# Kernel optimization log

Measured on AMD Instinct MI355X. Metric: run time of the kernel, lower is better.

Reference implementation:

```python
import jax, jax.numpy as jnp
import numpy as np

N = 50000   # nodes
E = 800000  # edges
F = 256     # input features
H = 256     # hidden units
L = 128     # n_labels
EPS = 1e-5


def setup_inputs():
    key = jax.random.key(0)
    ks = jax.random.split(key, 17)
    s = 0.05
    return {
        "features": jax.random.normal(ks[0], (N, F), jnp.float32),
        "edge_vals": jax.random.uniform(ks[1], (E,), jnp.float32),
        "W1": jax.random.normal(ks[2], (F, H), jnp.float32) * s,
        "db1": jax.random.normal(ks[3], (H,), jnp.float32) * s,
        "b1": jax.random.normal(ks[4], (H,), jnp.float32) * s,
        "g1": jax.random.uniform(ks[5], (H,), jnp.float32, 0.5, 1.5),
        "be1": jax.random.normal(ks[6], (H,), jnp.float32) * s,
        "W2": jax.random.normal(ks[7], (H, H), jnp.float32) * s,
        "b2": jax.random.normal(ks[8], (H,), jnp.float32) * s,
        "g2": jax.random.uniform(ks[9], (H,), jnp.float32, 0.5, 1.5),
        "be2": jax.random.normal(ks[10], (H,), jnp.float32) * s,
        "Wf": jax.random.normal(ks[11], (H, L), jnp.float32) * s,
        "bf": jax.random.normal(ks[12], (L,), jnp.float32) * s,
        "edge_rows": jax.random.randint(ks[13], (E,), 0, N, jnp.int32),
        "edge_cols": jax.random.randint(ks[14], (E,), 0, N, jnp.int32),
        "idx": jax.random.randint(ks[15], (N // 2,), 0, N, jnp.int32),
    }


def _spmm(edge_vals, rows, cols, x):
    # out[i] = sum_{(i,j) in E} A[i,j] * x[j]  (COO sparse @ dense)
    return jax.ops.segment_sum(edge_vals[:, None] * x[cols], rows, num_segments=N)


def _bn(x, gamma, beta):
    # training-mode BatchNormalization: batch (population) stats over nodes
    m = jnp.mean(x, axis=0)
    v = jnp.var(x, axis=0)
    return (x - m) * jax.lax.rsqrt(v + EPS) * gamma + beta


def reference(features, edge_vals, W1, db1, b1, g1, be1, W2, b2, g2, be2, Wf, bf,
              edge_rows, edge_cols, idx):
    # layer 1 (Dense has bias only for l == 0)
    h = features @ W1 + db1
    h = _spmm(edge_vals, edge_rows, edge_cols, h) + b1
    h = jax.nn.relu(_bn(h, g1, be1))
    # layer 2 (no dense bias)
    h = h @ W2
    h = _spmm(edge_vals, edge_rows, edge_cols, h) + b2
    h = jax.nn.relu(_bn(h, g2, be2))
    # dropout = identity (deterministic baseline); final dense head
    out = h @ Wf + bf
    return out[idx]
```

## Files before the change

### kernel.cpp

```cpp
#include <hip/hip_runtime.h>
#include <stdint.h>

#define NN 50000
#define EE 800000
#define FF 256
#define HH 256
#define LL 128
#define SBLK 1024

typedef __bf16 bf16x8 __attribute__((ext_vector_type(8)));
typedef float  f32x4  __attribute__((ext_vector_type(4)));

typedef __attribute__((address_space(1))) unsigned int uint_as1;
typedef __attribute__((address_space(3))) unsigned int uint_as3;

__device__ __forceinline__ unsigned short f2bf(float f) {
  union { float f; unsigned int u; } v; v.f = f;
  unsigned int u = v.u;
  u += 0x7FFFu + ((u >> 16) & 1u);
  return (unsigned short)(u >> 16);
}

__device__ __forceinline__ float bf2f(unsigned short u) {
  union { unsigned int u; float f; } v;
  v.u = ((unsigned int)u) << 16;
  return v.f;
}

__device__ __forceinline__ f32x4 bf4_to_f32(ushort4 u) {
  f32x4 r;
  r.x = bf2f(u.x); r.y = bf2f(u.y); r.z = bf2f(u.z); r.w = bf2f(u.w);
  return r;
}

__device__ __forceinline__ void gload_lds16(const void* g, void* l) {
  __builtin_amdgcn_global_load_lds((const uint_as1*)g, (uint_as3*)l, 16, 0, 0);
}

__global__ __launch_bounds__(256) void k_casts(const float* __restrict__ features,
                                               unsigned short* __restrict__ Xb,
                                               const float* __restrict__ W1,
                                               unsigned short* __restrict__ W1t,
                                               const float* __restrict__ W2,
                                               unsigned short* __restrict__ W2t,
                                               const float* __restrict__ Wf,
                                               unsigned short* __restrict__ Wft,
                                               int* __restrict__ cnt,
                                               int* __restrict__ statz) {
  __shared__ float tl[64 * 65];
  int b = blockIdx.x, t = threadIdx.x;
  if (b < 12500) {
    int i = b * 256 + t;
    f32x4 x = ((const f32x4*)features)[i];
    ushort4 o;
    o.x = f2bf(x.x); o.y = f2bf(x.y); o.z = f2bf(x.z); o.w = f2bf(x.w);
    ((ushort4*)Xb)[i] = o;
  } else if (b < 12540) {
    const float* in;
    unsigned short* out;
    int Nin, k0, n0;
    if (b < 12516) {
      in = W1; out = W1t; Nin = HH;
      int tt = b - 12500; k0 = (tt >> 2) * 64; n0 = (tt & 3) * 64;
    } else if (b < 12532) {
      in = W2; out = W2t; Nin = HH;
      int tt = b - 12516; k0 = (tt >> 2) * 64; n0 = (tt & 3) * 64;
    } else {
      in = Wf; out = Wft; Nin = LL;
      int tt = b - 12532; k0 = (tt >> 1) * 64; n0 = (tt & 1) * 64;
    }
#pragma unroll
    for (int j = 0; j < 16; ++j) {
      int idx = j * 256 + t;
      int r = idx >> 6, c = idx & 63;
      tl[r * 65 + c] = in[(size_t)(k0 + r) * Nin + n0 + c];
    }
    __syncthreads();
#pragma unroll
    for (int j = 0; j < 16; ++j) {
      int idx = j * 256 + t;
      int r = idx >> 6, c = idx & 63;
      out[(size_t)(n0 + r) * HH + k0 + c] = f2bf(tl[c * 65 + r]);
    }
  } else if (b < 12589) {
    int base = (b - 12540) * 1024 + t * 4;
    if (base + 3 < NN) {
      int4 z = {0, 0, 0, 0};
      *(int4*)(cnt + base) = z;
    } else {
      for (int j = 0; j < 4; ++j)
        if (base + j < NN) cnt[base + j] = 0;
    }
  } else {
    for (int i = t; i < 4 * HH + 64; i += 256) statz[i] = 0;
  }
}

__global__ __launch_bounds__(256) void k_hist(const int* __restrict__ rows,
                                              int* __restrict__ cnt, int E) {
  int i = blockIdx.x * 256 + threadIdx.x;
  if (i < E) atomicAdd(&cnt[rows[i]], 1);
}

__global__ __launch_bounds__(256) void k_alloc(const int* __restrict__ cnt,
                                               int* __restrict__ cursor,
                                               int* __restrict__ total, int n) {
  int i = blockIdx.x * 256 + threadIdx.x;
  int lane = threadIdx.x & 63;
  int c = (i < n) ? cnt[i] : 0;
  int incl = c;
#pragma unroll
  for (int off = 1; off < 64; off <<= 1) {
    int v = __shfl_up(incl, off, 64);
    if (lane >= off) incl += v;
  }
  int excl = incl - c;
  int wtot = __shfl(incl, 63, 64);
  int base = 0;
  if (lane == 0) base = atomicAdd(total, wtot);
  base = __shfl(base, 0, 64);
  if (i < n) cursor[i] = base + excl;
}

__global__ __launch_bounds__(256) void k_fill(const int* __restrict__ rows,
                                              const int* __restrict__ cols,
                                              const float* __restrict__ vals,
                                              int* __restrict__ cursor,
                                              unsigned int* __restrict__ csr, int E) {
  int i = (blockIdx.x * 256 + threadIdx.x) * 2;
  if (i + 1 < E) {
    int2 r2 = *(const int2*)(rows + i);
    int2 c2 = *(const int2*)(cols + i);
    float2 v2 = *(const float2*)(vals + i);
    int p0 = atomicAdd(&cursor[r2.x], 1);
    csr[p0] = ((unsigned int)c2.x << 16) | (unsigned int)f2bf(v2.x);
    int p1 = atomicAdd(&cursor[r2.y], 1);
    csr[p1] = ((unsigned int)c2.y << 16) | (unsigned int)f2bf(v2.y);
  } else if (i < E) {
    int p = atomicAdd(&cursor[rows[i]], 1);
    csr[p] = ((unsigned int)cols[i] << 16) | (unsigned int)f2bf(vals[i]);
  }
}

__global__ __launch_bounds__(256) void k_spmm(const unsigned short* __restrict__ X,
                                              const int* __restrict__ endp,
                                              const int* __restrict__ cnt,
                                              const unsigned int* __restrict__ csr,
                                              unsigned short* __restrict__ Y, int n) {
  int row = blockIdx.x * 4 + (threadIdx.x >> 6);
  int lane = threadIdx.x & 63;
  if (row >= n) return;
  int e = endp[row];
  int s = e - cnt[row];
  f32x4 a0 = {0.f, 0.f, 0.f, 0.f};
  f32x4 a1 = a0, a2 = a0, a3 = a0;
  int p = s;
  int e4 = s + ((e - s) & ~3);
  for (; p < e4; p += 4) {
    unsigned int c0 = csr[p + 0], c1 = csr[p + 1], c2 = csr[p + 2], c3 = csr[p + 3];
    ushort4 x0 = ((const ushort4*)(X + (size_t)(c0 >> 16) * HH))[lane];
    ushort4 x1 = ((const ushort4*)(X + (size_t)(c1 >> 16) * HH))[lane];
    ushort4 x2 = ((const ushort4*)(X + (size_t)(c2 >> 16) * HH))[lane];
    ushort4 x3 = ((const ushort4*)(X + (size_t)(c3 >> 16) * HH))[lane];
    a0 += bf2f((unsigned short)c0) * bf4_to_f32(x0);
    a1 += bf2f((unsigned short)c1) * bf4_to_f32(x1);
    a2 += bf2f((unsigned short)c2) * bf4_to_f32(x2);
    a3 += bf2f((unsigned short)c3) * bf4_to_f32(x3);
  }
  for (; p < e; ++p) {
    unsigned int c0 = csr[p];
    ushort4 x0 = ((const ushort4*)(X + (size_t)(c0 >> 16) * HH))[lane];
    a0 += bf2f((unsigned short)c0) * bf4_to_f32(x0);
  }
  f32x4 a = (a0 + a1) + (a2 + a3);
  ushort4 o;
  o.x = f2bf(a.x); o.y = f2bf(a.y); o.z = f2bf(a.z); o.w = f2bf(a.w);
  ((ushort4*)(Y + (size_t)row * HH))[lane] = o;
}

__global__ __launch_bounds__(256) void k_bnstats(const unsigned short* __restrict__ X,
                                                 float* __restrict__ part, int n) {
  __shared__ float red[4][64][9];
  const int w = threadIdx.x >> 6, l = threadIdx.x & 63;
  f32x4 s = {0.f, 0.f, 0.f, 0.f}, s2 = {0.f, 0.f, 0.f, 0.f};
  for (int r = blockIdx.x * 4 + w; r < n; r += gridDim.x * 4) {
    f32x4 v = bf4_to_f32(((const ushort4*)(X + (size_t)r * HH))[l]);
    s += v;
    s2 += v * v;
  }
#pragma unroll
  for (int j = 0; j < 4; ++j) { red[w][l][j] = s[j]; red[w][l][4 + j] = s2[j]; }
  __syncthreads();
  if (threadIdx.x < 64) {
    int ll = threadIdx.x;
#pragma unroll
    for (int j = 0; j < 8; ++j) {
      float v = red[0][ll][j] + red[1][ll][j] + red[2][ll][j] + red[3][ll][j];
      int c = ll * 4 + (j & 3);
      part[((j < 4) ? 0 : (SBLK * 256)) + blockIdx.x * 256 + c] = v;
    }
  }
}

__global__ __launch_bounds__(256) void k_bnred(const float* __restrict__ part,
                                               float* __restrict__ sums) {
  int c = threadIdx.x;
  int stat = blockIdx.x >> 3, chunk = blockIdx.x & 7;
  const float* p = part + stat * (SBLK * 256) + chunk * 128 * 256;
  float s0 = 0.f, s1 = 0.f, s2 = 0.f, s3 = 0.f;
  for (int b = 0; b < 128; b += 4) {
    s0 += p[(b + 0) * 256 + c];
    s1 += p[(b + 1) * 256 + c];
    s2 += p[(b + 2) * 256 + c];
    s3 += p[(b + 3) * 256 + c];
  }
  atomicAdd(&sums[stat * HH + c], (s0 + s1) + (s2 + s3));
}

__global__ __launch_bounds__(256) void k_bnrc(const unsigned short* __restrict__ X,
                                              const float* __restrict__ sums,
                                              const float* __restrict__ g,
                                              const float* __restrict__ be,
                                              unsigned short* __restrict__ out, int n4) {
  __shared__ float sc[HH], sh[HH];
  int t = threadIdx.x;
  {
    float inv = 1.f / (float)NN;
    float mean = sums[t] * inv;
    float var = sums[HH + t] * inv - mean * mean;
    float s = g[t] * rsqrtf(var + 1e-5f);
    sc[t] = s;
    sh[t] = be[t] - mean * s;
  }
  __syncthreads();
  for (int i = blockIdx.x * 256 + t; i < n4; i += gridDim.x * 256) {
    f32x4 x = bf4_to_f32(((const ushort4*)X)[i]);
    int c0 = (i * 4) & (HH - 1);
    ushort4 o;
    o.x = f2bf(fmaxf(x.x * sc[c0 + 0] + sh[c0 + 0], 0.f));
    o.y = f2bf(fmaxf(x.y * sc[c0 + 1] + sh[c0 + 1], 0.f));
    o.z = f2bf(fmaxf(x.z * sc[c0 + 2] + sh[c0 + 2], 0.f));
    o.w = f2bf(fmaxf(x.w * sc[c0 + 3] + sh[c0 + 3], 0.f));
    ((ushort4*)out)[i] = o;
  }
}

__global__ __launch_bounds__(256) void k_bnrc_pack(const unsigned short* __restrict__ X,
                                                   const float* __restrict__ sums,
                                                   const float* __restrict__ g,
                                                   const float* __restrict__ be,
                                                   const int* __restrict__ idx,
                                                   unsigned short* __restrict__ out) {
  __shared__ float sc[HH], sh[HH];
  int t = threadIdx.x;
  {
    float inv = 1.f / (float)NN;
    float mean = sums[t] * inv;
    float var = sums[HH + t] * inv - mean * mean;
    float s = g[t] * rsqrtf(var + 1e-5f);
    sc[t] = s;
    sh[t] = be[t] - mean * s;
  }
  __syncthreads();
  int i = blockIdx.x * 256 + t;
  int orow = i >> 6;
  int c0 = (i & 63) * 4;
  int irow = idx[orow];
  f32x4 x = bf4_to_f32(*(const ushort4*)(X + (size_t)irow * HH + c0));
  ushort4 o;
  o.x = f2bf(fmaxf(x.x * sc[c0 + 0] + sh[c0 + 0], 0.f));
  o.y = f2bf(fmaxf(x.y * sc[c0 + 1] + sh[c0 + 1], 0.f));
  o.z = f2bf(fmaxf(x.z * sc[c0 + 2] + sh[c0 + 2], 0.f));
  o.w = f2bf(fmaxf(x.w * sc[c0 + 3] + sh[c0 + 3], 0.f));
  ((ushort4*)out)[i] = o;
}

template <int OUTB>
__global__ __launch_bounds__(256, 3) void k_gemm(const unsigned short* __restrict__ A,
                                                 const unsigned short* __restrict__ Bt,
                                                 const float* __restrict__ bias,
                                                 void* __restrict__ Cv,
                                                 int M, int K, int Nn) {
  __shared__ unsigned short lA[128 * 64];
  __shared__ unsigned short lB[128 * 64];
  const int tid = threadIdx.x;
  const int wave = tid >> 6, lane = tid & 63;
  const int m0 = blockIdx.x * 128, n0 = blockIdx.y * 128;
  const int wm = (wave >> 1) * 64, wn = (wave & 1) * 64;
  const int lhi = lane >> 4, llo = lane & 15;

  const int srow = lane >> 3;
  const int scol = (lane & 7) * 8;
  const unsigned short *pA[4], *pB[4];
#pragma unroll
  for (int j = 0; j < 4; ++j) {
    int base = (wave * 4 + j) * 8 + srow;
    int ar = m0 + base;
    ar = ar < M ? ar : 0;
    pA[j] = A + (size_t)ar * K + scol;
    pB[j] = Bt + (size_t)(n0 + base) * K + scol;
  }

  f32x4 zero = {0.f, 0.f, 0.f, 0.f};
  f32x4 acc[4][4];
#pragma unroll
  for (int i = 0; i < 4; ++i)
#pragma unroll
    for (int j = 0; j < 4; ++j) acc[i][j] = zero;

  for (int k0 = 0; k0 < K; k0 += 64) {
#pragma unroll
    for (int j = 0; j < 4; ++j) {
      gload_lds16(pA[j] + k0, lA + (wave * 4 + j) * 8 * 64);
      gload_lds16(pB[j] + k0, lB + (wave * 4 + j) * 8 * 64);
    }
    __syncthreads();
    bf16x8 af[2][4], bfv[2][4];
#pragma unroll
    for (int ks = 0; ks < 2; ++ks) {
#pragma unroll
      for (int mt = 0; mt < 4; ++mt)
        af[ks][mt] = *(const bf16x8*)(lA + (wm + mt * 16 + llo) * 64 + ks * 32 + lhi * 8);
#pragma unroll
      for (int nt = 0; nt < 4; ++nt)
        bfv[ks][nt] = *(const bf16x8*)(lB + (wn + nt * 16 + llo) * 64 + ks * 32 + lhi * 8);
    }
#pragma unroll
    for (int ks = 0; ks < 2; ++ks)
#pragma unroll
      for (int mt = 0; mt < 4; ++mt)
#pragma unroll
        for (int nt = 0; nt < 4; ++nt)
          acc[mt][nt] = __builtin_amdgcn_mfma_f32_16x16x32_bf16(af[ks][mt], bfv[ks][nt], acc[mt][nt], 0, 0, 0);
    __syncthreads();
  }

#pragma unroll
  for (int nt = 0; nt < 4; ++nt) {
    int cn = n0 + wn + nt * 16 + llo;
    float bv = bias ? bias[cn] : 0.f;
#pragma unroll
    for (int mt = 0; mt < 4; ++mt) {
      int cm0 = m0 + wm + mt * 16 + lhi * 4;
#pragma unroll
      for (int r = 0; r < 4; ++r) {
        int cm = cm0 + r;
        if (cm < M) {
          float v = acc[mt][nt][r] + bv;
          if (OUTB)
            ((unsigned short*)Cv)[(size_t)cm * Nn + cn] = f2bf(v);
          else
            ((float*)Cv)[(size_t)cm * Nn + cn] = v;
        }
      }
    }
  }
}

extern "C" void kernel_launch(void* const* d_in, const int* in_sizes, int n_in,
                              void* d_out, int out_size, void* d_ws, size_t ws_size,
                              hipStream_t stream) {
  const float* features = (const float*)d_in[0];
  const float* edge_vals = (const float*)d_in[1];
  const float* W1 = (const float*)d_in[2];
  const float* db1 = (const float*)d_in[3];
  const float* g1 = (const float*)d_in[5];
  const float* be1 = (const float*)d_in[6];
  const float* W2 = (const float*)d_in[7];
  const float* g2 = (const float*)d_in[9];
  const float* be2 = (const float*)d_in[10];
  const float* Wf = (const float*)d_in[11];
  const float* bfb = (const float*)d_in[12];
  const int* erows = (const int*)d_in[13];
  const int* ecols = (const int*)d_in[14];
  const int* idx = (const int*)d_in[15];
  const int M3 = in_sizes[15];
  (void)n_in; (void)out_size; (void)ws_size;

  char* ws = (char*)d_ws;
  size_t off = 0;
  auto alloc = [&](size_t bytes) -> void* {
    void* p = (void*)(ws + off);
    off += (bytes + 255) & ~(size_t)255;
    return p;
  };
  unsigned short* Xb = (unsigned short*)alloc((size_t)NN * HH * 2);
  unsigned short* Ab = (unsigned short*)alloc((size_t)NN * HH * 2);
  unsigned short* Yb = (unsigned short*)alloc((size_t)NN * HH * 2);
  unsigned short* Pb = (unsigned short*)alloc((size_t)25000 * HH * 2);
  unsigned short* W1t = (unsigned short*)alloc((size_t)FF * HH * 2);
  unsigned short* W2t = (unsigned short*)alloc((size_t)HH * HH * 2);
  unsigned short* Wft = (unsigned short*)alloc((size_t)HH * LL * 2);
  int* cursor = (int*)alloc((size_t)NN * 4);
  int* cnt = (int*)alloc((size_t)NN * 4);
  unsigned int* csr = (unsigned int*)alloc((size_t)EE * 4);
  float* part = (float*)alloc((size_t)2 * SBLK * 256 * 4);
  float* stats = (float*)alloc(4 * HH * 4 + 256);
  float* sums1 = stats;
  float* sums2 = stats + 2 * HH;
  int* total = (int*)(stats + 4 * HH);

  k_casts<<<12590, 256, 0, stream>>>(features, Xb, W1, W1t, W2, W2t, Wf, Wft,
                                     cnt, (int*)stats);

  k_hist<<<(EE + 255) / 256, 256, 0, stream>>>(erows, cnt, EE);
  k_alloc<<<(NN + 255) / 256, 256, 0, stream>>>(cnt, cursor, total, NN);
  k_fill<<<(EE / 2 + 255) / 256, 256, 0, stream>>>(erows, ecols, edge_vals, cursor, csr, EE);

  k_gemm<1><<<dim3((NN + 127) / 128, HH / 128), 256, 0, stream>>>(Xb, W1t, db1, Ab, NN, FF, HH);
  k_spmm<<<(NN + 3) / 4, 256, 0, stream>>>(Ab, cursor, cnt, csr, Yb, NN);
  k_bnstats<<<SBLK, 256, 0, stream>>>(Yb, part, NN);
  k_bnred<<<16, 256, 0, stream>>>(part, sums1);
  k_bnrc<<<2048, 256, 0, stream>>>(Yb, sums1, g1, be1, Xb, NN * HH / 4);

  k_gemm<1><<<dim3((NN + 127) / 128, HH / 128), 256, 0, stream>>>(Xb, W2t, nullptr, Ab, NN, HH, HH);
  k_spmm<<<(NN + 3) / 4, 256, 0, stream>>>(Ab, cursor, cnt, csr, Yb, NN);
  k_bnstats<<<SBLK, 256, 0, stream>>>(Yb, part, NN);
  k_bnred<<<16, 256, 0, stream>>>(part, sums2);
  k_bnrc_pack<<<(M3 * 64) / 256, 256, 0, stream>>>(Yb, sums2, g2, be2, idx, Pb);

  k_gemm<0><<<dim3((M3 + 127) / 128, LL / 128), 256, 0, stream>>>(Pb, Wft, bfb, d_out, M3, HH, LL);
}
```

Measured before the change: 463.8 us.

## Fuse histogram into setup kernel and overlap CSR fill with layer-1 GEMM

The edge-row histogram moves into the cast/transpose setup kernel, and the zeroing of cnt and stats is replaced by hipMemsetAsync calls. The CSR fill is merged into the layer-1 GEMM launch: odd blocks scatter edges with a grid-stride loop while even blocks compute GEMM tiles. This cuts launch count and lets the atomic-bound scatter overlap the MFMA work. The risk is contention between the two block types and an interleaved block mapping that may hurt GEMM scheduling. The fill also loses its two-edges-per-thread vectorized loads.

```diff
diff --git a/kernel.cpp b/kernel.cpp
--- a/kernel.cpp
+++ b/kernel.cpp
@@ -37,37 +37,41 @@
   __builtin_amdgcn_global_load_lds((const uint_as1*)g, (uint_as3*)l, 16, 0, 0);
 }
 
-__global__ __launch_bounds__(256) void k_casts(const float* __restrict__ features,
+__global__ __launch_bounds__(256) void k_setup(const int* __restrict__ erows,
+                                               int* __restrict__ cnt,
+                                               const float* __restrict__ features,
                                                unsigned short* __restrict__ Xb,
                                                const float* __restrict__ W1,
                                                unsigned short* __restrict__ W1t,
                                                const float* __restrict__ W2,
                                                unsigned short* __restrict__ W2t,
                                                const float* __restrict__ Wf,
-                                               unsigned short* __restrict__ Wft,
-                                               int* __restrict__ cnt,
-                                               int* __restrict__ statz) {
+                                               unsigned short* __restrict__ Wft) {
   __shared__ float tl[64 * 65];
   int b = blockIdx.x, t = threadIdx.x;
-  if (b < 12500) {
+  if (b < 3125) {
     int i = b * 256 + t;
+    if (i < EE) atomicAdd(&cnt[erows[i]], 1);
+  } else if (b < 15625) {
+    int i = (b - 3125) * 256 + t;
     f32x4 x = ((const f32x4*)features)[i];
     ushort4 o;
     o.x = f2bf(x.x); o.y = f2bf(x.y); o.z = f2bf(x.z); o.w = f2bf(x.w);
     ((ushort4*)Xb)[i] = o;
-  } else if (b < 12540) {
+  } else {
+    int tt = b - 15625;
     const float* in;
     unsigned short* out;
     int Nin, k0, n0;
-    if (b < 12516) {
+    if (tt < 16) {
       in = W1; out = W1t; Nin = HH;
-      int tt = b - 12500; k0 = (tt >> 2) * 64; n0 = (tt & 3) * 64;
-    } else if (b < 12532) {
+      k0 = (tt >> 2) * 64; n0 = (tt & 3) * 64;
+    } else if (tt < 32) {
       in = W2; out = W2t; Nin = HH;
-      int tt = b - 12516; k0 = (tt >> 2) * 64; n0 = (tt & 3) * 64;
+      tt -= 16; k0 = (tt >> 2) * 64; n0 = (tt & 3) * 64;
     } else {
       in = Wf; out = Wft; Nin = LL;
-      int tt = b - 12532; k0 = (tt >> 1) * 64; n0 = (tt & 1) * 64;
+      tt -= 32; k0 = (tt >> 1) * 64; n0 = (tt & 1) * 64;
     }
 #pragma unroll
     for (int j = 0; j < 16; ++j) {
@@ -82,24 +86,7 @@
       int r = idx >> 6, c = idx & 63;
       out[(size_t)(n0 + r) * HH + k0 + c] = f2bf(tl[c * 65 + r]);
     }
-  } else if (b < 12589) {
-    int base = (b - 12540) * 1024 + t * 4;
-    if (base + 3 < NN) {
-      int4 z = {0, 0, 0, 0};
-      *(int4*)(cnt + base) = z;
-    } else {
-      for (int j = 0; j < 4; ++j)
-        if (base + j < NN) cnt[base + j] = 0;
-    }
-  } else {
-    for (int i = t; i < 4 * HH + 64; i += 256) statz[i] = 0;
-  }
-}
-
-__global__ __launch_bounds__(256) void k_hist(const int* __restrict__ rows,
-                                              int* __restrict__ cnt, int E) {
-  int i = blockIdx.x * 256 + threadIdx.x;
-  if (i < E) atomicAdd(&cnt[rows[i]], 1);
+  }
 }
 
 __global__ __launch_bounds__(256) void k_alloc(const int* __restrict__ cnt,
@@ -122,23 +109,88 @@
   if (i < n) cursor[i] = base + excl;
 }
 
-__global__ __launch_bounds__(256) void k_fill(const int* __restrict__ rows,
-                                              const int* __restrict__ cols,
-                                              const float* __restrict__ vals,
-                                              int* __restrict__ cursor,
-                                              unsigned int* __restrict__ csr, int E) {
-  int i = (blockIdx.x * 256 + threadIdx.x) * 2;
-  if (i + 1 < E) {
-    int2 r2 = *(const int2*)(rows + i);
-    int2 c2 = *(const int2*)(cols + i);
-    float2 v2 = *(const float2*)(vals + i);
-    int p0 = atomicAdd(&cursor[r2.x], 1);
-    csr[p0] = ((unsigned int)c2.x << 16) | (unsigned int)f2bf(v2.x);
-    int p1 = atomicAdd(&cursor[r2.y], 1);
-    csr[p1] = ((unsigned int)c2.y << 16) | (unsigned int)f2bf(v2.y);
-  } else if (i < E) {
-    int p = atomicAdd(&cursor[rows[i]], 1);
-    csr[p] = ((unsigned int)cols[i] << 16) | (unsigned int)f2bf(vals[i]);
+__global__ __launch_bounds__(256, 3) void k_l1(const unsigned short* __restrict__ A,
+                                               const unsigned short* __restrict__ Bt,
+                                               const float* __restrict__ bias,
+                                               unsigned short* __restrict__ C,
+                                               int M, int K, int Nn,
+                                               const int* __restrict__ rows,
+                                               const int* __restrict__ cols,
+                                               const float* __restrict__ vals,
+                                               int* __restrict__ cursor,
+                                               unsigned int* __restrict__ csr, int E) {
+  __shared__ unsigned short lA[128 * 64];
+  __shared__ unsigned short lB[128 * 64];
+  const int b = blockIdx.x;
+  const int tid = threadIdx.x;
+  if (b & 1) {
+    for (int i = (b >> 1) * 256 + tid; i < E; i += 782 * 256) {
+      int p = atomicAdd(&cursor[rows[i]], 1);
+      csr[p] = ((unsigned int)cols[i] << 16) | (unsigned int)f2bf(vals[i]);
+    }
+    return;
+  }
+  const int gb = b >> 1;
+  const int m0 = (gb % 391) * 128, n0 = (gb / 391) * 128;
+  const int wave = tid >> 6, lane = tid & 63;
+  const int wm = (wave >> 1) * 64, wn = (wave & 1) * 64;
+  const int lhi = lane >> 4, llo = lane & 15;
+  const int srow = lane >> 3;
+  const int scol = (lane & 7) * 8;
+  const unsigned short *pA[4], *pB[4];
+#pragma unroll
+  for (int j = 0; j < 4; ++j) {
+    int base = (wave * 4 + j) * 8 + srow;
+    int ar = m0 + base;
+    ar = ar < M ? ar : 0;
+    pA[j] = A + (size_t)ar * K + scol;
+    pB[j] = Bt + (size_t)(n0 + base) * K + scol;
+  }
+  f32x4 zero = {0.f, 0.f, 0.f, 0.f};
+  f32x4 acc[4][4];
+#pragma unroll
+  for (int i = 0; i < 4; ++i)
+#pragma unroll
+    for (int j = 0; j < 4; ++j) acc[i][j] = zero;
+  for (int k0 = 0; k0 < K; k0 += 64) {
+#pragma unroll
+    for (int j = 0; j < 4; ++j) {
+      gload_lds16(pA[j] + k0, lA + (wave * 4 + j) * 8 * 64);
+      gload_lds16(pB[j] + k0, lB + (wave * 4 + j) * 8 * 64);
+    }
+    __syncthreads();
+    bf16x8 af[2][4], bfv[2][4];
+#pragma unroll
+    for (int ks = 0; ks < 2; ++ks) {
+#pragma unroll
+      for (int mt = 0; mt < 4; ++mt)
+        af[ks][mt] = *(const bf16x8*)(lA + (wm + mt * 16 + llo) * 64 + ks * 32 + lhi * 8);
+#pragma unroll
+      for (int nt = 0; nt < 4; ++nt)
+        bfv[ks][nt] = *(const bf16x8*)(lB + (wn + nt * 16 + llo) * 64 + ks * 32 + lhi * 8);
+    }
+#pragma unroll
+    for (int ks = 0; ks < 2; ++ks)
+#pragma unroll
+      for (int mt = 0; mt < 4; ++mt)
+#pragma unroll
+        for (int nt = 0; nt < 4; ++nt)
+          acc[mt][nt] = __builtin_amdgcn_mfma_f32_16x16x32_bf16(af[ks][mt], bfv[ks][nt], acc[mt][nt], 0, 0, 0);
+    __syncthreads();
+  }
+#pragma unroll
+  for (int nt = 0; nt < 4; ++nt) {
+    int cn = n0 + wn + nt * 16 + llo;
+    float bv = bias[cn];
+#pragma unroll
+    for (int mt = 0; mt < 4; ++mt) {
+      int cm0 = m0 + wm + mt * 16 + lhi * 4;
+#pragma unroll
+      for (int r = 0; r < 4; ++r) {
+        int cm = cm0 + r;
+        if (cm < M) C[(size_t)cm * Nn + cn] = f2bf(acc[mt][nt][r] + bv);
+      }
+    }
   }
 }
 
@@ -288,7 +340,6 @@
   const int m0 = blockIdx.x * 128, n0 = blockIdx.y * 128;
   const int wm = (wave >> 1) * 64, wn = (wave & 1) * 64;
   const int lhi = lane >> 4, llo = lane & 15;
-
   const int srow = lane >> 3;
   const int scol = (lane & 7) * 8;
   const unsigned short *pA[4], *pB[4];
@@ -300,14 +351,12 @@
     pA[j] = A + (size_t)ar * K + scol;
     pB[j] = Bt + (size_t)(n0 + base) * K + scol;
   }
-
   f32x4 zero = {0.f, 0.f, 0.f, 0.f};
   f32x4 acc[4][4];
 #pragma unroll
   for (int i = 0; i < 4; ++i)
 #pragma unroll
     for (int j = 0; j < 4; ++j) acc[i][j] = zero;
-
   for (int k0 = 0; k0 < K; k0 += 64) {
 #pragma unroll
     for (int j = 0; j < 4; ++j) {
@@ -334,7 +383,6 @@
           acc[mt][nt] = __builtin_amdgcn_mfma_f32_16x16x32_bf16(af[ks][mt], bfv[ks][nt], acc[mt][nt], 0, 0, 0);
     __syncthreads();
   }
-
 #pragma unroll
   for (int nt = 0; nt < 4; ++nt) {
     int cn = n0 + wn + nt * 16 + llo;
@@ -400,14 +448,14 @@
   float* sums2 = stats + 2 * HH;
   int* total = (int*)(stats + 4 * HH);
 
-  k_casts<<<12590, 256, 0, stream>>>(features, Xb, W1, W1t, W2, W2t, Wf, Wft,
-                                     cnt, (int*)stats);
-
-  k_hist<<<(EE + 255) / 256, 256, 0, stream>>>(erows, cnt, EE);
+  hipMemsetAsync(cnt, 0, (size_t)NN * 4, stream);
+  hipMemsetAsync(stats, 0, 4 * HH * 4 + 256, stream);
+
+  k_setup<<<15665, 256, 0, stream>>>(erows, cnt, features, Xb, W1, W1t, W2, W2t, Wf, Wft);
   k_alloc<<<(NN + 255) / 256, 256, 0, stream>>>(cnt, cursor, total, NN);
-  k_fill<<<(EE / 2 + 255) / 256, 256, 0, stream>>>(erows, ecols, edge_vals, cursor, csr, EE);
-
-  k_gemm<1><<<dim3((NN + 127) / 128, HH / 128), 256, 0, stream>>>(Xb, W1t, db1, Ab, NN, FF, HH);
+
+  k_l1<<<1564, 256, 0, stream>>>(Xb, W1t, db1, Ab, NN, FF, HH,
+                                 erows, ecols, edge_vals, cursor, csr, EE);
   k_spmm<<<(NN + 3) / 4, 256, 0, stream>>>(Ab, cursor, cnt, csr, Yb, NN);
   k_bnstats<<<SBLK, 256, 0, stream>>>(Yb, part, NN);
   k_bnred<<<16, 256, 0, stream>>>(part, sums1);
```

Result: faster. 433.8 us (-6.5%).
